# Kernel optimization log

Measured on AMD Instinct MI355X. Metric: run time of the kernel, lower is better.

## Reference

```python
import jax, jax.numpy as jnp
import numpy as np

HEAD = 16  # from init_kwargs
NEG_FILL = -1e20


def setup_inputs() -> dict:
    key = jax.random.key(0)
    ks = jax.random.split(key, 6)
    N, S, E = 4, 2048, 1024
    D = E // HEAD  # 64
    value = jax.random.normal(ks[0], (N, S, E), dtype=jnp.float32)
    key_t = jax.random.normal(ks[1], (N, S, E), dtype=jnp.float32)
    query = jax.random.normal(ks[2], (N, S, E), dtype=jnp.float32)
    # multiplicative causal mask broadcastable to (N, H, S, S)
    mask = jnp.tril(jnp.ones((S, S), dtype=jnp.float32))[None, None, :, :]
    # per-head-dim projection weights (Dense(head_dim) applied after reshape,
    # so weights are (D, D), shared across heads) -- faithful to source
    sc = 1.0 / np.sqrt(D)
    Wq = jax.random.normal(ks[3], (D, D), dtype=jnp.float32) * sc
    Wk = jax.random.normal(ks[4], (D, D), dtype=jnp.float32) * sc
    Wv = jax.random.normal(ks[5], (D, D), dtype=jnp.float32) * sc
    return {"value": value, "key": key_t, "query": query, "mask": mask,
            "Wq": Wq, "Wk": Wk, "Wv": Wv}


def reference(value, key, query, mask, Wq, Wk, Wv):
    N, Lq, E = query.shape
    H = HEAD
    D = E // H
    # reshape to heads, then project last dim (D -> D)
    q = jnp.einsum('nqhd,de->nqhe', query.reshape(N, Lq, H, D), Wq)
    k = jnp.einsum('nkhd,de->nkhe', key.reshape(N, key.shape[1], H, D), Wk)
    v = jnp.einsum('nvhd,de->nvhe', value.reshape(N, value.shape[1], H, D), Wv)
    # unscaled QK^T (source has no 1/sqrt(d))
    energy = jnp.einsum('nqhd,nkhd->nhqk', q, k)  # (N,H,Lq,Lk)
    energy = energy * mask
    energy = jnp.where(energy == 0, NEG_FILL, energy)
    attention = jax.nn.softmax(energy, axis=-1)
    out = jnp.einsum('nhql,nlhd->nqhd', attention, v).reshape(N, Lq, H * D)
    return out  # fc_layer defined in __init__ but never used in call()
```

## Files before the change

### kernel.cpp

```cpp
#include <hip/hip_runtime.h>
#include <hip/hip_bf16.h>
#include <math.h>


#define NB  4
#define SEQ 2048
#define HD  16
#define DH  64
#define NH  (NB*HD)

typedef _Float16 half8  __attribute__((ext_vector_type(8)));
typedef _Float16 half2  __attribute__((ext_vector_type(2)));
typedef __fp16   fp16x2 __attribute__((ext_vector_type(2)));
typedef float    f32x4  __attribute__((ext_vector_type(4)));
typedef float    f32x16 __attribute__((ext_vector_type(16)));

__device__ inline half2 pkrtz(float a, float b) {
  union { fp16x2 f; half2 h; } u;
  u.f = __builtin_amdgcn_cvt_pkrtz(a, b);
  return u.h;
}

__device__ inline void gload16(const void* g, void* l) {
  __builtin_amdgcn_global_load_lds(
      (const __attribute__((address_space(1))) void*)g,
      (__attribute__((address_space(3))) void*)l, 16, 0, 0);
}

__global__ __launch_bounds__(256) void proj_kernel(
    const float* __restrict__ q_in, const float* __restrict__ k_in,
    const float* __restrict__ v_in,
    const float* __restrict__ Wq, const float* __restrict__ Wk,
    const float* __restrict__ Wv,
    _Float16* __restrict__ Qp, _Float16* __restrict__ Kp,
    _Float16* __restrict__ Vt)
{
  __shared__ float Wl[64*64];
  const int t = threadIdx.x;
  const int which = blockIdx.z;
  const float* in = which == 0 ? q_in : (which == 1 ? k_in : v_in);
  const float* W  = which == 0 ? Wq   : (which == 1 ? Wk   : Wv);

  const int nh = blockIdx.y;
  const int n = nh >> 4, h = nh & 15;
  const int s0 = blockIdx.x * 256;

  #pragma unroll
  for (int i = 0; i < 16; ++i) Wl[i*256 + t] = W[i*256 + t];
  __syncthreads();

  const int w = t >> 6, lane = t & 63, lr = lane & 15, lg = lane >> 4;

  if (which < 2) {
    const float oscale = (which == 0) ? 1.44269504088896f : 1.0f;
    half8 bfr[4][2];
    #pragma unroll
    for (int g = 0; g < 4; ++g)
      #pragma unroll
      for (int kc = 0; kc < 2; ++kc)
        #pragma unroll
        for (int i = 0; i < 8; ++i)
          bfr[g][kc][i] = (_Float16)Wl[(kc*32 + lg*8 + i)*64 + 16*g + lr];

    _Float16* outp = (which == 0 ? Qp : Kp) + (size_t)nh*SEQ*DH;
    #pragma unroll
    for (int pass = 0; pass < 4; ++pass) {
      int row0 = s0 + (pass*4 + w)*16;
      const float* ip = in + ((size_t)(n*SEQ + row0 + lr))*(HD*DH) + h*DH;
      float4 a0 = *(const float4*)(ip + lg*8);
      float4 a1 = *(const float4*)(ip + lg*8 + 4);
      float4 a2 = *(const float4*)(ip + 32 + lg*8);
      float4 a3 = *(const float4*)(ip + 32 + lg*8 + 4);
      half8 af0, af1;
      af0[0]=(_Float16)a0.x; af0[1]=(_Float16)a0.y; af0[2]=(_Float16)a0.z; af0[3]=(_Float16)a0.w;
      af0[4]=(_Float16)a1.x; af0[5]=(_Float16)a1.y; af0[6]=(_Float16)a1.z; af0[7]=(_Float16)a1.w;
      af1[0]=(_Float16)a2.x; af1[1]=(_Float16)a2.y; af1[2]=(_Float16)a2.z; af1[3]=(_Float16)a2.w;
      af1[4]=(_Float16)a3.x; af1[5]=(_Float16)a3.y; af1[6]=(_Float16)a3.z; af1[7]=(_Float16)a3.w;
      f32x4 c[4] = {{0,0,0,0},{0,0,0,0},{0,0,0,0},{0,0,0,0}};
      #pragma unroll
      for (int g = 0; g < 4; ++g) {
        c[g] = __builtin_amdgcn_mfma_f32_16x16x32_f16(af0, bfr[g][0], c[g], 0, 0, 0);
        c[g] = __builtin_amdgcn_mfma_f32_16x16x32_f16(af1, bfr[g][1], c[g], 0, 0, 0);
      }
      #pragma unroll
      for (int g = 0; g < 4; ++g)
        #pragma unroll
        for (int j = 0; j < 4; ++j)
          outp[(size_t)(row0 + 4*lg + j)*DH + 16*g + lr] =
              (_Float16)(c[g][j] * oscale);
    }
  } else {
    half8 afr[2];
    #pragma unroll
    for (int kc = 0; kc < 2; ++kc)
      #pragma unroll
      for (int i = 0; i < 8; ++i)
        afr[kc][i] = (_Float16)Wl[(kc*32 + lg*8 + i)*64 + w*16 + lr];

    _Float16* outp = Vt + (size_t)nh*DH*SEQ;
    #pragma unroll
    for (int pass = 0; pass < 4; ++pass) {
      int sc0 = s0 + pass*64;
      f32x4 c[4] = {{0,0,0,0},{0,0,0,0},{0,0,0,0},{0,0,0,0}};
      #pragma unroll
      for (int g = 0; g < 4; ++g) {
        const float* ip = in + ((size_t)(n*SEQ + sc0 + 16*g + lr))*(HD*DH) + h*DH;
        float4 b0 = *(const float4*)(ip + lg*8);
        float4 b1 = *(const float4*)(ip + lg*8 + 4);
        float4 b2 = *(const float4*)(ip + 32 + lg*8);
        float4 b3 = *(const float4*)(ip + 32 + lg*8 + 4);
        half8 bf0, bf1;
        bf0[0]=(_Float16)b0.x; bf0[1]=(_Float16)b0.y; bf0[2]=(_Float16)b0.z; bf0[3]=(_Float16)b0.w;
        bf0[4]=(_Float16)b1.x; bf0[5]=(_Float16)b1.y; bf0[6]=(_Float16)b1.z; bf0[7]=(_Float16)b1.w;
        bf1[0]=(_Float16)b2.x; bf1[1]=(_Float16)b2.y; bf1[2]=(_Float16)b2.z; bf1[3]=(_Float16)b2.w;
        bf1[4]=(_Float16)b3.x; bf1[5]=(_Float16)b3.y; bf1[6]=(_Float16)b3.z; bf1[7]=(_Float16)b3.w;
        c[g] = __builtin_amdgcn_mfma_f32_16x16x32_f16(afr[0], bf0, c[g], 0, 0, 0);
        c[g] = __builtin_amdgcn_mfma_f32_16x16x32_f16(afr[1], bf1, c[g], 0, 0, 0);
      }
      #pragma unroll
      for (int g = 0; g < 4; ++g)
        #pragma unroll
        for (int j = 0; j < 4; ++j) {
          int kcol = 16*g + lr;
          int pcol = (kcol & ~12) | ((kcol & 8) >> 1) | ((kcol & 4) << 1);
          outp[(size_t)(w*16 + 4*lg + j)*SEQ + sc0 + pcol] = (_Float16)c[g][j];
        }
    }
  }
}

#define STAGE(kd, vd, ktn)                                        \
  do {                                                            \
    gload16(kg + (size_t)(ktn)*DH, (kd) + tid*8);                 \
    gload16(kg + (size_t)(ktn)*DH + 32*DH, (kd) + (256+tid)*8);   \
    gload16(vg + (ktn), (vd) + tid*8);                            \
    gload16(vg + (ktn) + 32*SEQ, (vd) + (256+tid)*8);             \
  } while (0)

__global__ __launch_bounds__(256) void attn_kernel(
    const _Float16* __restrict__ Qp,
    const _Float16* __restrict__ Kp,
    const _Float16* __restrict__ Vt,
    float* __restrict__ out)
{
  __shared__ __attribute__((aligned(16))) _Float16 Kl[2][64*64];
  __shared__ __attribute__((aligned(16))) _Float16 Vl[2][64*64];

  const int head = blockIdx.y;
  const int n = head >> 4, h = head & 15;
  const int p  = blockIdx.x;
  const int tid = threadIdx.x;
  const int w = tid >> 6, lane = tid & 63;
  const int lq = lane & 31, lg1 = lane >> 5;

  const int TmaxA = 2*p + 1;
  const int TmaxB = 31 - 2*p;
  const int q0A = p*128 + w*32;
  const int q0B = (15 - p)*128 + w*32;
  const int TwA = q0A >> 6;
  const int TwB = q0B >> 6;
  const int G   = TmaxA + TmaxB + 2;

  const _Float16* Kbase = Kp + (size_t)head*SEQ*DH;
  const _Float16* Vbase = Vt + (size_t)head*DH*SEQ;

  const _Float16* QrowA = Qp + ((size_t)head*SEQ + q0A + lq)*DH + 8*lg1;
  const _Float16* QrowB = Qp + ((size_t)head*SEQ + q0B + lq)*DH + 8*lg1;
  half8 qf[4];
  #pragma unroll
  for (int c = 0; c < 4; ++c) qf[c] = *(const half8*)(QrowA + 16*c);

  int roff[2][4];
  #pragma unroll
  for (int rt = 0; rt < 2; ++rt)
    #pragma unroll
    for (int c = 0; c < 4; ++c)
      roff[rt][c] = (32*rt + lq)*128 + (((2*c + lg1) ^ (lq & 7)) << 4);

  const int srow = tid >> 3;
  const int scs  = (tid & 7) ^ (srow & 7);
  const _Float16* kg = Kbase + (size_t)srow*DH + scs*8;
  const _Float16* vg = Vbase + (size_t)srow*SEQ + scs*8;

  float m = -INFINITY, lsum = 0.f;
  f32x16 o0 = {0,0,0,0,0,0,0,0,0,0,0,0,0,0,0,0};
  f32x16 o1 = {0,0,0,0,0,0,0,0,0,0,0,0,0,0,0,0};

  STAGE(&Kl[0][0], &Vl[0][0], 0);

  int cur = 0;
  for (int g = 0; g < G; ++g) {
    const bool phA = (g <= TmaxA);
    const int  tt  = phA ? g : (g - TmaxA - 1);
    const int  Tw  = phA ? TwA : TwB;

    if (g + 1 < G) {
      const int gn  = g + 1;
      const int ktn = (gn <= TmaxA ? gn : (gn - TmaxA - 1)) * 64;
      STAGE(&Kl[cur^1][0], &Vl[cur^1][0], ktn);
      asm volatile("s_waitcnt vmcnt(4)" ::: "memory");
    } else {
      asm volatile("s_waitcnt vmcnt(0)" ::: "memory");
    }
    __builtin_amdgcn_sched_barrier(0);
    __builtin_amdgcn_s_barrier();
    __builtin_amdgcn_sched_barrier(0);

    if (tt <= Tw) {
      const char* Kb = (const char*)&Kl[cur][0];
      const char* Vb = (const char*)&Vl[cur][0];
      const int kt = tt*64;
      const int q  = (phA ? q0A : q0B) + lq;

      f32x16 s0 = {0,0,0,0,0,0,0,0,0,0,0,0,0,0,0,0};
      f32x16 s1 = {0,0,0,0,0,0,0,0,0,0,0,0,0,0,0,0};
      __builtin_amdgcn_s_setprio(1);
      #pragma unroll
      for (int c = 0; c < 4; ++c) {
        half8 ka = *(const half8*)(Kb + roff[0][c]);
        half8 kb = *(const half8*)(Kb + roff[1][c]);
        s0 = __builtin_amdgcn_mfma_f32_32x32x16_f16(ka, qf[c], s0, 0, 0, 0);
        s1 = __builtin_amdgcn_mfma_f32_32x32x16_f16(kb, qf[c], s1, 0, 0, 0);
      }
      __builtin_amdgcn_s_setprio(0);
      if (tt == Tw) {
        #pragma unroll
        for (int j = 0; j < 16; ++j) {
          int kl = 4*lg1 + 8*(j>>2) + (j&3);
          if (kt + kl      > q) s0[j] = -1e30f;
          if (kt + 32 + kl > q) s1[j] = -1e30f;
        }
      }
      float t0[8];
      #pragma unroll
      for (int j = 0; j < 8; ++j)
        t0[j] = fmaxf(fmaxf(s0[j], s0[j+8]), fmaxf(s1[j], s1[j+8]));
      float pm = fmaxf(fmaxf(fmaxf(t0[0],t0[1]), fmaxf(t0[2],t0[3])),
                       fmaxf(fmaxf(t0[4],t0[5]), fmaxf(t0[6],t0[7])));
      pm = fmaxf(pm, __shfl_xor(pm, 32));
      if (!__all(pm <= m + 8.f)) {
        float mn = fmaxf(m, pm);
        float sc = exp2f(m - mn);
        m = mn;
        lsum *= sc;
        #pragma unroll
        for (int j = 0; j < 16; ++j) { o0[j] *= sc; o1[j] *= sc; }
      }
      #pragma unroll
      for (int j = 0; j < 16; ++j) {
        s0[j] = exp2f(s0[j] - m);
        s1[j] = exp2f(s1[j] - m);
      }
      float u0[8];
      #pragma unroll
      for (int j = 0; j < 8; ++j)
        u0[j] = (s0[j] + s0[j+8]) + (s1[j] + s1[j+8]);
      float ps = ((u0[0]+u0[1]) + (u0[2]+u0[3])) + ((u0[4]+u0[5]) + (u0[6]+u0[7]));
      ps += __shfl_xor(ps, 32);
      lsum += ps;

      half2 pkA[8], pkB[8];
      #pragma unroll
      for (int jj = 0; jj < 8; ++jj) {
        pkA[jj] = pkrtz(s0[2*jj], s0[2*jj+1]);
        pkB[jj] = pkrtz(s1[2*jj], s1[2*jj+1]);
      }
      __builtin_amdgcn_s_setprio(1);
      #pragma unroll
      for (int c = 0; c < 4; ++c) {
        union { half8 hh; half2 pp[4]; } pb;
        pb.pp[0] = (c < 2) ? pkA[(c&1)*4 + 0] : pkB[(c&1)*4 + 0];
        pb.pp[1] = (c < 2) ? pkA[(c&1)*4 + 1] : pkB[(c&1)*4 + 1];
        pb.pp[2] = (c < 2) ? pkA[(c&1)*4 + 2] : pkB[(c&1)*4 + 2];
        pb.pp[3] = (c < 2) ? pkA[(c&1)*4 + 3] : pkB[(c&1)*4 + 3];
        half8 va = *(const half8*)(Vb + roff[0][c]);
        half8 vb = *(const half8*)(Vb + roff[1][c]);
        o0 = __builtin_amdgcn_mfma_f32_32x32x16_f16(va, pb.hh, o0, 0, 0, 0);
        o1 = __builtin_amdgcn_mfma_f32_32x32x16_f16(vb, pb.hh, o1, 0, 0, 0);
      }
      __builtin_amdgcn_s_setprio(0);
    }

    __builtin_amdgcn_sched_barrier(0);
    __builtin_amdgcn_s_barrier();

    if (g == TmaxA) {
      float inv = 1.0f / lsum;
      float* orow = out + ((size_t)n*SEQ + q0A + lq)*(HD*DH) + h*DH;
      #pragma unroll
      for (int j = 0; j < 16; ++j) {
        int dl = 4*lg1 + 8*(j>>2) + (j&3);
        orow[dl]      = o0[j] * inv;
        orow[32 + dl] = o1[j] * inv;
      }
      m = -INFINITY; lsum = 0.f;
      #pragma unroll
      for (int j = 0; j < 16; ++j) { o0[j] = 0.f; o1[j] = 0.f; }
      #pragma unroll
      for (int c = 0; c < 4; ++c) qf[c] = *(const half8*)(QrowB + 16*c);
    }
    cur ^= 1;
  }

  float inv = 1.0f / lsum;
  float* orow = out + ((size_t)n*SEQ + q0B + lq)*(HD*DH) + h*DH;
  #pragma unroll
  for (int j = 0; j < 16; ++j) {
    int dl = 4*lg1 + 8*(j>>2) + (j&3);
    orow[dl]      = o0[j] * inv;
    orow[32 + dl] = o1[j] * inv;
  }
}

extern "C" void kernel_launch(void* const* d_in, const int* in_sizes, int n_in,
                              void* d_out, int out_size, void* d_ws, size_t ws_size,
                              hipStream_t stream) {
  (void)in_sizes; (void)n_in; (void)out_size; (void)ws_size;
  const float* value = (const float*)d_in[0];
  const float* key   = (const float*)d_in[1];
  const float* query = (const float*)d_in[2];
  const float* Wq = (const float*)d_in[4];
  const float* Wk = (const float*)d_in[5];
  const float* Wv = (const float*)d_in[6];

  _Float16* Qp = (_Float16*)d_ws;
  _Float16* Kp = Qp + (size_t)NH*SEQ*DH;
  _Float16* Vt = Kp + (size_t)NH*SEQ*DH;
  float* out = (float*)d_out;

  proj_kernel<<<dim3(8, 64, 3), 256, 0, stream>>>(query, key, value,
                                                  Wq, Wk, Wv, Qp, Kp, Vt);
  attn_kernel<<<dim3(8, 64), 256, 0, stream>>>(Qp, Kp, Vt, out);
}
```

Measured before the change: 126.4 us.

## Split KV tiles across two wave groups per block and merge softmax partials

Doubles the block to 512 threads as two 4-wave groups. Each group processes alternating KV tiles of the same query rows with its own double-buffered LDS stage, and the two partial softmax states (m, l, O) are merged through LDS at each output point. This roughly halves the serial KV loop length per block and raises wave count per CU to expose more parallelism. In exchange it adds an LDS merge with extra barriers, fp16 rounding of one partial output, double the LDS footprint, and load imbalance when one group's tile is masked out.

```diff
diff --git a/kernel.cpp b/kernel.cpp
--- a/kernel.cpp
+++ b/kernel.cpp
@@ -129,37 +129,86 @@
   }
 }
 
-#define STAGE(kd, vd, ktn)                                        \
+#define STAGEG(buf, ktn)                                          \
   do {                                                            \
-    gload16(kg + (size_t)(ktn)*DH, (kd) + tid*8);                 \
-    gload16(kg + (size_t)(ktn)*DH + 32*DH, (kd) + (256+tid)*8);   \
-    gload16(vg + (ktn), (vd) + tid*8);                            \
-    gload16(vg + (ktn) + 32*SEQ, (vd) + (256+tid)*8);             \
+    _Float16* kd = &lds[buf][g][0][0];                            \
+    _Float16* vd = &lds[buf][g][1][0];                            \
+    gload16(kg + (size_t)(ktn)*DH,         kd + gtid*8);          \
+    gload16(kg + (size_t)(ktn)*DH + 32*DH, kd + (256+gtid)*8);    \
+    gload16(vg + (ktn),                    vd + gtid*8);          \
+    gload16(vg + (ktn) + 32*SEQ,           vd + (256+gtid)*8);    \
   } while (0)
 
-__global__ __launch_bounds__(256) void attn_kernel(
+#define MERGE_OUT(Q0W)                                                      \
+  do {                                                                      \
+    unsigned* ov = (unsigned*)&lds[cur][0][0][0];                           \
+    float invl = lsum > 0.f ? 1.f/lsum : 0.f;                               \
+    if (g == 1) {                                                           \
+      unsigned* pp = ov + (wi*64 + lane)*18;                                \
+      _Pragma("unroll")                                                     \
+      for (int jj = 0; jj < 8; ++jj) {                                      \
+        union { half2 h; unsigned u; } u0, u1;                              \
+        u0.h = pkrtz(o0[2*jj]*invl, o0[2*jj+1]*invl);                       \
+        u1.h = pkrtz(o1[2*jj]*invl, o1[2*jj+1]*invl);                       \
+        pp[jj] = u0.u; pp[8+jj] = u1.u;                                     \
+      }                                                                     \
+      union { float f; unsigned u; } um, ul;                                \
+      um.f = m; ul.f = lsum;                                                \
+      pp[16] = um.u; pp[17] = ul.u;                                         \
+    }                                                                       \
+    __syncthreads();                                                        \
+    if (g == 0) {                                                           \
+      const unsigned* pp = ov + (wi*64 + lane)*18;                          \
+      union { float f; unsigned u; } um, ul;                                \
+      um.u = pp[16]; ul.u = pp[17];                                         \
+      float m1 = um.f, l1 = ul.f;                                           \
+      float mf = fmaxf(m, m1);                                              \
+      float wa = lsum * exp2f(m - mf);                                      \
+      float wb = (l1 > 0.f ? l1 : 0.f) * exp2f(m1 - mf);                    \
+      float invd = 1.f / (wa + wb);                                         \
+      float ca = wa * invl * invd;                                          \
+      float cb = wb * invd;                                                 \
+      float* orow = out + ((size_t)n*SEQ + (Q0W) + lq)*(HD*DH) + h*DH;      \
+      _Pragma("unroll")                                                     \
+      for (int jj = 0; jj < 8; ++jj) {                                      \
+        union { unsigned u; half2 h; } v0, v1;                              \
+        v0.u = pp[jj]; v1.u = pp[8+jj];                                     \
+        int j0 = 2*jj, j1 = 2*jj + 1;                                       \
+        int dl0 = 4*lg1 + 8*(j0>>2) + (j0&3);                               \
+        int dl1 = 4*lg1 + 8*(j1>>2) + (j1&3);                               \
+        orow[dl0]      = ca*o0[j0] + cb*(float)v0.h[0];                     \
+        orow[dl1]      = ca*o0[j1] + cb*(float)v0.h[1];                     \
+        orow[32 + dl0] = ca*o1[j0] + cb*(float)v1.h[0];                     \
+        orow[32 + dl1] = ca*o1[j1] + cb*(float)v1.h[1];                     \
+      }                                                                     \
+    }                                                                       \
+    __syncthreads();                                                        \
+  } while (0)
+
+__global__ __launch_bounds__(512, 4) void attn_kernel(
     const _Float16* __restrict__ Qp,
     const _Float16* __restrict__ Kp,
     const _Float16* __restrict__ Vt,
     float* __restrict__ out)
 {
-  __shared__ __attribute__((aligned(16))) _Float16 Kl[2][64*64];
-  __shared__ __attribute__((aligned(16))) _Float16 Vl[2][64*64];
+  __shared__ __attribute__((aligned(16))) _Float16 lds[2][2][2][4096];
 
   const int head = blockIdx.y;
   const int n = head >> 4, h = head & 15;
   const int p  = blockIdx.x;
   const int tid = threadIdx.x;
-  const int w = tid >> 6, lane = tid & 63;
+  const int w8 = tid >> 6;
+  const int g  = w8 >> 2;
+  const int wi = w8 & 3;
+  const int lane = tid & 63;
   const int lq = lane & 31, lg1 = lane >> 5;
+  const int gtid = tid & 255;
 
   const int TmaxA = 2*p + 1;
-  const int TmaxB = 31 - 2*p;
-  const int q0A = p*128 + w*32;
-  const int q0B = (15 - p)*128 + w*32;
-  const int TwA = q0A >> 6;
-  const int TwB = q0B >> 6;
-  const int G   = TmaxA + TmaxB + 2;
+  const int q0A = p*128 + wi*32;
+  const int q0B = (15 - p)*128 + wi*32;
+  const int TwA = (q0A >> 6);
+  const int TwB = (q0B >> 6);
 
   const _Float16* Kbase = Kp + (size_t)head*SEQ*DH;
   const _Float16* Vbase = Vt + (size_t)head*DH*SEQ;
@@ -177,8 +226,8 @@
     for (int c = 0; c < 4; ++c)
       roff[rt][c] = (32*rt + lq)*128 + (((2*c + lg1) ^ (lq & 7)) << 4);
 
-  const int srow = tid >> 3;
-  const int scs  = (tid & 7) ^ (srow & 7);
+  const int srow = gtid >> 3;
+  const int scs  = (gtid & 7) ^ (srow & 7);
   const _Float16* kg = Kbase + (size_t)srow*DH + scs*8;
   const _Float16* vg = Vbase + (size_t)srow*SEQ + scs*8;
 
@@ -186,18 +235,14 @@
   f32x16 o0 = {0,0,0,0,0,0,0,0,0,0,0,0,0,0,0,0};
   f32x16 o1 = {0,0,0,0,0,0,0,0,0,0,0,0,0,0,0,0};
 
-  STAGE(&Kl[0][0], &Vl[0][0], 0);
+  STAGEG(0, g*64);
 
   int cur = 0;
-  for (int g = 0; g < G; ++g) {
-    const bool phA = (g <= TmaxA);
-    const int  tt  = phA ? g : (g - TmaxA - 1);
-    const int  Tw  = phA ? TwA : TwB;
-
-    if (g + 1 < G) {
-      const int gn  = g + 1;
-      const int ktn = (gn <= TmaxA ? gn : (gn - TmaxA - 1)) * 64;
-      STAGE(&Kl[cur^1][0], &Vl[cur^1][0], ktn);
+  for (int i = 0; i <= 16; ++i) {
+    if (i < 16) {
+      const int Gn  = 2*(i + 1) + g;
+      const int ktn = (Gn <= TmaxA ? Gn : Gn - TmaxA - 1) * 64;
+      STAGEG(cur^1, ktn);
       asm volatile("s_waitcnt vmcnt(4)" ::: "memory");
     } else {
       asm volatile("s_waitcnt vmcnt(0)" ::: "memory");
@@ -206,9 +251,14 @@
     __builtin_amdgcn_s_barrier();
     __builtin_amdgcn_sched_barrier(0);
 
+    const int G    = 2*i + g;
+    const bool phA = (G <= TmaxA);
+    const int  tt  = phA ? G : G - TmaxA - 1;
+    const int  Tw  = phA ? TwA : TwB;
+
     if (tt <= Tw) {
-      const char* Kb = (const char*)&Kl[cur][0];
-      const char* Vb = (const char*)&Vl[cur][0];
+      const char* Kb = (const char*)&lds[cur][g][0][0];
+      const char* Vb = (const char*)&lds[cur][g][1][0];
       const int kt = tt*64;
       const int q  = (phA ? q0A : q0B) + lq;
 
@@ -284,32 +334,18 @@
     __builtin_amdgcn_sched_barrier(0);
     __builtin_amdgcn_s_barrier();
 
-    if (g == TmaxA) {
-      float inv = 1.0f / lsum;
-      float* orow = out + ((size_t)n*SEQ + q0A + lq)*(HD*DH) + h*DH;
-      #pragma unroll
-      for (int j = 0; j < 16; ++j) {
-        int dl = 4*lg1 + 8*(j>>2) + (j&3);
-        orow[dl]      = o0[j] * inv;
-        orow[32 + dl] = o1[j] * inv;
-      }
+    if (i == p) {
+      MERGE_OUT(q0A);
       m = -INFINITY; lsum = 0.f;
       #pragma unroll
       for (int j = 0; j < 16; ++j) { o0[j] = 0.f; o1[j] = 0.f; }
       #pragma unroll
       for (int c = 0; c < 4; ++c) qf[c] = *(const half8*)(QrowB + 16*c);
     }
-    cur ^= 1;
+    if (i < 16) cur ^= 1;
   }
 
-  float inv = 1.0f / lsum;
-  float* orow = out + ((size_t)n*SEQ + q0B + lq)*(HD*DH) + h*DH;
-  #pragma unroll
-  for (int j = 0; j < 16; ++j) {
-    int dl = 4*lg1 + 8*(j>>2) + (j&3);
-    orow[dl]      = o0[j] * inv;
-    orow[32 + dl] = o1[j] * inv;
-  }
+  MERGE_OUT(q0B);
 }
 
 extern "C" void kernel_launch(void* const* d_in, const int* in_sizes, int n_in,
@@ -330,5 +366,5 @@
 
   proj_kernel<<<dim3(8, 64, 3), 256, 0, stream>>>(query, key, value,
                                                   Wq, Wk, Wv, Qp, Kp, Vt);
-  attn_kernel<<<dim3(8, 64), 256, 0, stream>>>(Qp, Kp, Vt, out);
-}
+  attn_kernel<<<dim3(8, 64), 512, 0, stream>>>(Qp, Kp, Vt, out);
+}
```

After: 110.0 us. 13.0% less time.
